# Kernel tuning notes

Hardware: AMD Instinct MI355X
Metric: run time of the kernel (lower is better)

The kernel has to match this reference:

```python
import jax, jax.numpy as jnp
import numpy as np

EPS = 1e-5

def _conv(x, w):
    # 3x3, stride 1, pad 1, NCHW/OIHW
    return jax.lax.conv_general_dilated(x, w, (1, 1), ((1, 1), (1, 1)),
                                        dimension_numbers=('NCHW', 'OIHW', 'NCHW'))

def _bn(x, g, b, m, v):
    inv = jax.lax.rsqrt(v + EPS)
    return (x - m[None, :, None, None]) * (g * inv)[None, :, None, None] + b[None, :, None, None]

def _hardtanh(x):
    return jnp.clip(x, -1.0, 1.0)

def _binarize(x):
    # sign binarization with straight-through estimator (identity gradient)
    s = jnp.where(x >= 0, 1.0, -1.0).astype(x.dtype)
    return x + jax.lax.stop_gradient(s - x)

def _maxpool2(x):
    return jax.lax.reduce_window(x, -jnp.inf, jax.lax.max, (1, 1, 2, 2), (1, 1, 2, 2), 'VALID')

def setup_inputs() -> dict:
    key = jax.random.key(0)
    ks = jax.random.split(key, 8)
    c1, c3, c5 = 128 * 3, 256 * 3, 512 * 3  # infl_ratio = 3
    def W(k, o, i):
        return jax.random.normal(k, (o, i, 3, 3), jnp.float32) * 0.05
    inp = {}
    inp['x'] = jax.random.normal(ks[0], (128, 3, 32, 32), jnp.float32)
    inp['w1'] = W(ks[1], c1, 3)
    inp['w2'] = W(ks[2], c1, c1)
    inp['w3'] = W(ks[3], c3, c1)
    inp['w4'] = W(ks[4], c3, c3)
    inp['w5'] = W(ks[5], c5, c3)
    inp['w6'] = W(ks[6], 512, c5)
    for i, c in zip(range(1, 7), [c1, c1, c3, c3, c5, 512]):
        inp['bn%d_g' % i] = jnp.ones((c,), jnp.float32)
        inp['bn%d_b' % i] = jnp.zeros((c,), jnp.float32)
        inp['bn%d_m' % i] = jnp.zeros((c,), jnp.float32)
        inp['bn%d_v' % i] = jnp.ones((c,), jnp.float32)
    inp['w_lin'] = jax.random.normal(ks[7], (10, 512 * 4 * 4), jnp.float32) * 0.02
    return inp

def reference(x, w1, w2, w3, w4, w5, w6,
              bn1_g, bn1_b, bn1_m, bn1_v,
              bn2_g, bn2_b, bn2_m, bn2_v,
              bn3_g, bn3_b, bn3_m, bn3_v,
              bn4_g, bn4_b, bn4_m, bn4_v,
              bn5_g, bn5_b, bn5_m, bn5_v,
              bn6_g, bn6_b, bn6_m, bn6_v,
              w_lin):
    # block 1: full-precision conv
    h = _hardtanh(_bn(_conv(x, w1), bn1_g, bn1_b, bn1_m, bn1_v))
    # block 2: binarized conv -> maxpool -> BN -> hardtanh
    h = _conv(_binarize(h), _binarize(w2))
    h = _hardtanh(_bn(_maxpool2(h), bn2_g, bn2_b, bn2_m, bn2_v))
    # block 3
    h = _conv(_binarize(h), _binarize(w3))
    h = _hardtanh(_bn(h, bn3_g, bn3_b, bn3_m, bn3_v))
    # block 4
    h = _conv(_binarize(h), _binarize(w4))
    h = _hardtanh(_bn(_maxpool2(h), bn4_g, bn4_b, bn4_m, bn4_v))
    # block 5
    h = _conv(_binarize(h), _binarize(w5))
    h = _hardtanh(_bn(h, bn5_g, bn5_b, bn5_m, bn5_v))
    # block 6
    h = _conv(_binarize(h), _binarize(w6))
    h = _hardtanh(_bn(_maxpool2(h), bn6_g, bn6_b, bn6_m, bn6_v))
    # classifier
    h = h.reshape(-1, 512 * 4 * 4)
    logits = h @ w_lin.T
    return jax.nn.log_softmax(logits, axis=-1)
```

## Files before the change

kernel.cpp:

```cpp
#include <hip/hip_runtime.h>
#include <stdint.h>

#define EPS 1e-5f

typedef __attribute__((ext_vector_type(4))) int i32x4;

__global__ __launch_bounds__(384) void conv1_a1_kernel(
    const float* __restrict__ x,
    const float* __restrict__ w1,
    const float* __restrict__ g,
    const float* __restrict__ b,
    const float* __restrict__ m,
    const float* __restrict__ v,
    char* __restrict__ a1)
{
    const int bid = blockIdx.x;
    const int n = bid >> 2;
    const int q = bid & 3;
    const int tid = threadIdx.x;

    __shared__ float xin[3][10][34];

    const int y0 = q * 8;
    for (int idx = tid; idx < 3 * 10 * 34; idx += 384) {
        int xx = idx % 34;
        int yy = (idx / 34) % 10;
        int ci = idx / 340;
        int gy = y0 - 1 + yy, gx = xx - 1;
        float val = 0.f;
        if (gy >= 0 && gy < 32 && gx >= 0 && gx < 32)
            val = x[((n * 3 + ci) * 32 + gy) * 32 + gx];
        xin[ci][yy][xx] = val;
    }

    float wr[27];
    {
        const float* wp = w1 + tid * 27;
#pragma unroll
        for (int i = 0; i < 27; ++i) wr[i] = wp[i];
    }
    const float scale = g[tid] * rsqrtf(v[tid] + EPS);
    const float mean = m[tid], beta = b[tid];
    __syncthreads();

    for (int yy = 0; yy < 8; ++yy) {
        const int gy = y0 + yy;
        char* orow = a1 + ((size_t)(n * 34 + gy + 1) * 34 + 1) * 384 + tid;
#pragma unroll
        for (int xp = 0; xp < 32; xp += 2) {
            float a0 = 0.f, a1v = 0.f;
#pragma unroll
            for (int ci = 0; ci < 3; ++ci)
#pragma unroll
                for (int dy = 0; dy < 3; ++dy) {
                    float c0 = xin[ci][yy + dy][xp];
                    float c1 = xin[ci][yy + dy][xp + 1];
                    float c2 = xin[ci][yy + dy][xp + 2];
                    float c3 = xin[ci][yy + dy][xp + 3];
                    const float* wrow = &wr[(ci * 3 + dy) * 3];
                    a0 += c0 * wrow[0] + c1 * wrow[1] + c2 * wrow[2];
                    a1v += c1 * wrow[0] + c2 * wrow[1] + c3 * wrow[2];
                }
            float t0 = (a0 - mean) * scale + beta;
            float t1 = (a1v - mean) * scale + beta;
            orow[(size_t)xp * 384] = (t0 >= 0.f) ? 1 : -1;
            orow[(size_t)(xp + 1) * 384] = (t1 >= 0.f) ? 1 : -1;
        }
    }
}

__global__ void pack_bp_kernel(const float* __restrict__ w,
                               char* __restrict__ bp, int Co, int Ci)
{
    int KC = Ci >> 6;
    int idx = blockIdx.x * 256 + threadIdx.x;
    int total = Co * 9 * Ci;
    if (idx >= total) return;
    int t  = idx & 15;
    int fg = (idx >> 4) & 3;
    int co = (idx >> 6) % Co;
    int s  = idx / (Co * 64);
    int tap = s / KC, kc = s % KC;
    int ci = kc * 64 + fg * 16 + t;
    bp[idx] = (w[((size_t)co * Ci + ci) * 9 + tap] >= 0.f) ? 1 : -1;
}

template<int Ci, int Co, int H, int W, int WM, int GN, bool POOL, bool OUTF32>
__global__ __launch_bounds__(WM * 128, 4) void gemm_fused_kernel(
    const char* __restrict__ A,
    const char* __restrict__ Bp,
    const float* __restrict__ g, const float* __restrict__ b,
    const float* __restrict__ m, const float* __restrict__ v,
    char* __restrict__ aout, float* __restrict__ fout)
{
    constexpr int T   = WM * 128;
    constexpr int TM  = WM * 64;
    constexpr int KC  = Ci / 64;
    constexpr int S   = 9 * KC;
    constexpr int WP  = W + 2;
    constexpr int GM  = (128 * H * W) / TM;
    constexpr int BU  = 512 / T;
    constexpr int HO  = POOL ? H / 2 : H;
    constexpr int WO  = POOL ? W / 2 : W;

    __shared__ __align__(16) char lsA[2][TM * 64];
    __shared__ __align__(16) char lsB[2][128 * 64];

    const int id = blockIdx.x;
    const int xcd = id & 7;
    const int s0 = id >> 3;
    const int bm = xcd * (GM / 8) + s0 / GN;
    const int bn = s0 % GN;

    const int tid = threadIdx.x;
    const int lane = tid & 63;
    const int wave = tid >> 6;
    const int wm = wave >> 1, wn = wave & 1;
    const int fr = lane & 15, fg = lane >> 4;

    const int pl = tid >> 1, h = tid & 1;
    int gm = bm * TM + pl;
    int n_  = gm / (H * W);
    int rr = gm % (H * W);
    int y_  = rr / W, x_ = rr % W;
    const char* abase = A + ((size_t)(n_ * (H + 2) + y_) * WP + x_) * Ci + h * 32;
    const int xsw = (pl >> 1) & 3;
    const int wa0 = pl * 64 + (((2 * h) ^ xsw) << 4);
    const int wa1 = pl * 64 + (((2 * h + 1) ^ xsw) << 4);

    const char* bbase = Bp + (size_t)bn * 128 * 64;
    int bdst[BU];
#pragma unroll
    for (int q = 0; q < BU; ++q) {
        int u = tid + q * T;
        int col = u >> 2, sl = u & 3;
        bdst[q] = col * 64 + ((sl ^ ((col >> 1) & 3)) << 4);
    }
    const size_t bstep = (size_t)Co * 64;

    int raA[4];
#pragma unroll
    for (int i = 0; i < 4; ++i) {
        int row = wm * 64 + i * 16 + fr;
        raA[i] = row * 64 + ((fg ^ ((row >> 1) & 3)) << 4);
    }
    int raB[4];
#pragma unroll
    for (int j = 0; j < 4; ++j) {
        int col = wn * 64 + j * 16 + fr;
        raB[j] = col * 64 + ((fg ^ ((col >> 1) & 3)) << 4);
    }

    i32x4 acc[4][4] = {};

    {
        *reinterpret_cast<uint4*>(&lsA[0][wa0]) =
            *reinterpret_cast<const uint4*>(abase);
        *reinterpret_cast<uint4*>(&lsA[0][wa1]) =
            *reinterpret_cast<const uint4*>(abase + 16);
#pragma unroll
        for (int q = 0; q < BU; ++q)
            *reinterpret_cast<uint4*>(&lsB[0][bdst[q]]) =
                *reinterpret_cast<const uint4*>(bbase + (tid + q * T) * 16);
    }
    __syncthreads();

    for (int s = 0; s < S; ++s) {
        const int cur = s & 1;
        const bool more = (s + 1 < S);

        uint4 av0, av1, bst[BU];
        if (more) {
            int s1 = s + 1;
            int tap = s1 / KC, kc = s1 % KC;
            const char* src = abase + ((tap / 3) * WP + (tap % 3)) * Ci + kc * 64;
            av0 = *reinterpret_cast<const uint4*>(src);
            av1 = *reinterpret_cast<const uint4*>(src + 16);
            const char* bsrc = bbase + (size_t)s1 * bstep;
#pragma unroll
            for (int q = 0; q < BU; ++q)
                bst[q] = *reinterpret_cast<const uint4*>(bsrc + (tid + q * T) * 16);
        }

        i32x4 af[4], bf[4];
#pragma unroll
        for (int i = 0; i < 4; ++i)
            af[i] = *reinterpret_cast<const i32x4*>(&lsA[cur][raA[i]]);
#pragma unroll
        for (int j = 0; j < 4; ++j)
            bf[j] = *reinterpret_cast<const i32x4*>(&lsB[cur][raB[j]]);
#pragma unroll
        for (int i = 0; i < 4; ++i)
#pragma unroll
            for (int j = 0; j < 4; ++j)
                acc[i][j] = __builtin_amdgcn_mfma_i32_16x16x64_i8(
                    af[i], bf[j], acc[i][j], 0, 0, 0);

        if (more) {
            *reinterpret_cast<uint4*>(&lsA[cur ^ 1][wa0]) = av0;
            *reinterpret_cast<uint4*>(&lsA[cur ^ 1][wa1]) = av1;
#pragma unroll
            for (int q = 0; q < BU; ++q)
                *reinterpret_cast<uint4*>(&lsB[cur ^ 1][bdst[q]]) = bst[q];
        }
        __syncthreads();
    }

    int colj[4];
    float sc[4], mn[4], bt[4];
#pragma unroll
    for (int j = 0; j < 4; ++j) {
        colj[j] = bn * 128 + wn * 64 + j * 16 + fr;
        sc[j] = g[colj[j]] * rsqrtf(v[colj[j]] + EPS);
        mn[j] = m[colj[j]];
        bt[j] = b[colj[j]];
    }

    if constexpr (POOL && W == 32) {
        const int n = bm >> 2;
        const int Y = 4 * (bm & 3) + wm;
#pragma unroll
        for (int ip = 0; ip < 2; ++ip)
#pragma unroll
            for (int rp = 0; rp < 2; ++rp) {
                int X = ip * 8 + fg * 2 + rp;
#pragma unroll
                for (int j = 0; j < 4; ++j) {
                    int val = max(max(acc[ip][j][2 * rp], acc[ip][j][2 * rp + 1]),
                                  max(acc[ip + 2][j][2 * rp], acc[ip + 2][j][2 * rp + 1]));
                    float t = ((float)val - mn[j]) * sc[j] + bt[j];
                    aout[((size_t)(n * (HO + 2) + Y + 1) * (WO + 2) + X + 1) * Co + colj[j]]
                        = (t >= 0.f) ? 1 : -1;
                }
            }
    } else if constexpr (POOL && W == 16) {
        const int n = bm;
#pragma unroll
        for (int iv = 0; iv < 2; ++iv) {
            int Y = wm * 2 + iv;
#pragma unroll
            for (int rp = 0; rp < 2; ++rp) {
                int X = fg * 2 + rp;
#pragma unroll
                for (int j = 0; j < 4; ++j) {
                    int val = max(max(acc[2 * iv][j][2 * rp], acc[2 * iv][j][2 * rp + 1]),
                                  max(acc[2 * iv + 1][j][2 * rp], acc[2 * iv + 1][j][2 * rp + 1]));
                    float t = ((float)val - mn[j]) * sc[j] + bt[j];
                    aout[((size_t)(n * (HO + 2) + Y + 1) * (WO + 2) + X + 1) * Co + colj[j]]
                        = (t >= 0.f) ? 1 : -1;
                }
            }
        }
    } else if constexpr (POOL && W == 8) {
        const int n = bm * 2 + wm;
#pragma unroll
        for (int i = 0; i < 4; ++i)
#pragma unroll
            for (int rp = 0; rp < 2; ++rp)
#pragma unroll
                for (int j = 0; j < 4; ++j) {
                    int hm = max(acc[i][j][2 * rp], acc[i][j][2 * rp + 1]);
                    int other = __shfl_xor(hm, 32);
                    int val = max(hm, other);
                    if (fg < 2) {
                        int X = (fg & 1) * 2 + rp;
                        float t = ((float)val - mn[j]) * sc[j] + bt[j];
                        t = fminf(1.f, fmaxf(-1.f, t));
                        fout[((size_t)(n * Co + colj[j]) * 4 + i) * 4 + X] = t;
                    }
                }
    } else if constexpr (!POOL && W == 16) {
        const int n = bm;
#pragma unroll
        for (int i = 0; i < 4; ++i) {
            int y = wm * 4 + i;
#pragma unroll
            for (int r = 0; r < 4; ++r) {
                int x = fg * 4 + r;
#pragma unroll
                for (int j = 0; j < 4; ++j) {
                    float t = ((float)acc[i][j][r] - mn[j]) * sc[j] + bt[j];
                    aout[((size_t)(n * (H + 2) + y + 1) * (W + 2) + x + 1) * Co + colj[j]]
                        = (t >= 0.f) ? 1 : -1;
                }
            }
        }
    } else {
        const int n = bm * 2 + wm;
#pragma unroll
        for (int i = 0; i < 4; ++i) {
            int y = 2 * i + (fg >> 1);
#pragma unroll
            for (int r = 0; r < 4; ++r) {
                int x = (fg & 1) * 4 + r;
#pragma unroll
                for (int j = 0; j < 4; ++j) {
                    float t = ((float)acc[i][j][r] - mn[j]) * sc[j] + bt[j];
                    aout[((size_t)(n * (H + 2) + y + 1) * (W + 2) + x + 1) * Co + colj[j]]
                        = (t >= 0.f) ? 1 : -1;
                }
            }
        }
    }
}

__global__ void classifier_kernel(const float* __restrict__ h,
                                  const float* __restrict__ wl,
                                  float* __restrict__ out)
{
    int n = blockIdx.x;
    int tid = threadIdx.x;
    float acc[10];
#pragma unroll
    for (int j = 0; j < 10; ++j) acc[j] = 0.f;
    for (int k = tid; k < 8192; k += 256) {
        float hv = h[n * 8192 + k];
#pragma unroll
        for (int j = 0; j < 10; ++j) acc[j] += hv * wl[j * 8192 + k];
    }
    __shared__ float sred[256];
    __shared__ float logit[10];
    for (int j = 0; j < 10; ++j) {
        sred[tid] = acc[j];
        __syncthreads();
        for (int s = 128; s > 0; s >>= 1) {
            if (tid < s) sred[tid] += sred[tid + s];
            __syncthreads();
        }
        if (tid == 0) logit[j] = sred[0];
        __syncthreads();
    }
    if (tid == 0) {
        float mx = logit[0];
#pragma unroll
        for (int j = 1; j < 10; ++j) mx = fmaxf(mx, logit[j]);
        float s = 0.f;
#pragma unroll
        for (int j = 0; j < 10; ++j) s += expf(logit[j] - mx);
        float lse = logf(s) + mx;
#pragma unroll
        for (int j = 0; j < 10; ++j) out[n * 10 + j] = logit[j] - lse;
    }
}

extern "C" void kernel_launch(void* const* d_in, const int* in_sizes, int n_in,
                              void* d_out, int out_size, void* d_ws, size_t ws_size,
                              hipStream_t stream)
{
    const float* x    = (const float*)d_in[0];
    const float* w1   = (const float*)d_in[1];
    const float* w2   = (const float*)d_in[2];
    const float* w3   = (const float*)d_in[3];
    const float* w4   = (const float*)d_in[4];
    const float* w5   = (const float*)d_in[5];
    const float* w6   = (const float*)d_in[6];
    const float* bn_g[6], *bn_b[6], *bn_m[6], *bn_v[6];
    for (int i = 0; i < 6; ++i) {
        bn_g[i] = (const float*)d_in[7 + i * 4 + 0];
        bn_b[i] = (const float*)d_in[7 + i * 4 + 1];
        bn_m[i] = (const float*)d_in[7 + i * 4 + 2];
        bn_v[i] = (const float*)d_in[7 + i * 4 + 3];
    }
    const float* wlin = (const float*)d_in[31];
    float* out = (float*)d_out;

    const size_t A1 = (size_t)128 * 34 * 34 * 384;
    const size_t A2 = (size_t)128 * 18 * 18 * 384;
    const size_t A3 = (size_t)128 * 18 * 18 * 768;
    const size_t A4 = (size_t)128 * 10 * 10 * 768;
    const size_t A5 = (size_t)128 * 10 * 10 * 1536;
    const size_t SB = A2;
    const size_t SC = A3;
    const size_t H6 = (size_t)128 * 8192 * 4;

    char* ws = (char*)d_ws;
    auto alloc = [&](size_t bytes) {
        char* p = ws;
        ws += (bytes + 255) & ~(size_t)255;
        return p;
    };
    char*  a1 = (char*)alloc(A1);
    char*  sb = (char*)alloc(SB);
    char*  scs = (char*)alloc(SC);
    float* h6 = (float*)alloc(H6);
    char* bp2 = (char*)alloc((size_t)(9 * 6 + 1) * 384 * 64);
    char* bp3 = (char*)alloc((size_t)(9 * 6 + 1) * 768 * 64);
    char* bp4 = (char*)alloc((size_t)(9 * 12 + 1) * 768 * 64);
    char* bp5 = (char*)alloc((size_t)(9 * 12 + 1) * 1536 * 64);
    char* bp6 = (char*)alloc((size_t)(9 * 24 + 1) * 512 * 64);

    char* a2 = sb;
    char* a3 = scs;
    char* a4 = sb;
    char* a5 = scs;

    {
        int t;
        t = 384 * 9 * 384;
        pack_bp_kernel<<<(t + 255) / 256, 256, 0, stream>>>(w2, bp2, 384, 384);
        t = 768 * 9 * 384;
        pack_bp_kernel<<<(t + 255) / 256, 256, 0, stream>>>(w3, bp3, 768, 384);
        t = 768 * 9 * 768;
        pack_bp_kernel<<<(t + 255) / 256, 256, 0, stream>>>(w4, bp4, 768, 768);
        t = 1536 * 9 * 768;
        pack_bp_kernel<<<(t + 255) / 256, 256, 0, stream>>>(w5, bp5, 1536, 768);
        t = 512 * 9 * 1536;
        pack_bp_kernel<<<(t + 255) / 256, 256, 0, stream>>>(w6, bp6, 512, 1536);
    }

    hipMemsetAsync(a1, 0, A1, stream);
    conv1_a1_kernel<<<128 * 4, 384, 0, stream>>>(
        x, w1, bn_g[0], bn_b[0], bn_m[0], bn_v[0], a1);

    hipMemsetAsync(a2, 0, A2, stream);
    gemm_fused_kernel<384, 384, 32, 32, 4, 3, true, false>
        <<<512 * 3, 512, 0, stream>>>(a1, bp2, bn_g[1], bn_b[1], bn_m[1], bn_v[1],
                                      a2, nullptr);
    hipMemsetAsync(a3, 0, A3, stream);
    gemm_fused_kernel<384, 768, 16, 16, 4, 6, false, false>
        <<<128 * 6, 512, 0, stream>>>(a2, bp3, bn_g[2], bn_b[2], bn_m[2], bn_v[2],
                                      a3, nullptr);
    hipMemsetAsync(a4, 0, A4, stream);
    gemm_fused_kernel<768, 768, 16, 16, 4, 6, true, false>
        <<<128 * 6, 512, 0, stream>>>(a3, bp4, bn_g[3], bn_b[3], bn_m[3], bn_v[3],
                                      a4, nullptr);
    hipMemsetAsync(a5, 0, A5, stream);
    gemm_fused_kernel<768, 1536, 8, 8, 2, 12, false, false>
        <<<64 * 12, 256, 0, stream>>>(a4, bp5, bn_g[4], bn_b[4], bn_m[4], bn_v[4],
                                      a5, nullptr);
    gemm_fused_kernel<1536, 512, 8, 8, 2, 4, true, true>
        <<<64 * 4, 256, 0, stream>>>(a5, bp6, bn_g[5], bn_b[5], bn_m[5], bn_v[5],
                                     nullptr, h6);

    classifier_kernel<<<128, 256, 0, stream>>>(h6, wlin, out);
}
```

Measured before the change: 884.1 us.

## Add taller per-wave int8 MFMA GEMM kernel for conv layers 2-4

Adds a new implicit-GEMM kernel in which each of four waves computes a 128x64 output sub-tile (8x4 MFMA fragments) instead of 64x64, keeping the 256x128 block tile but with 256 threads instead of 512. Each wave reuses its B fragments across more A rows, cutting LDS reads per MFMA. The cost is a larger accumulator file (128 VGPRs for acc), with launch bounds relaxed to 2 blocks per CU, and new epilogue index mappings for pooled and unpooled outputs.

```diff
diff --git a/kernel.cpp b/kernel.cpp
--- a/kernel.cpp
+++ b/kernel.cpp
@@ -85,6 +85,195 @@
     bp[idx] = (w[((size_t)co * Ci + ci) * 9 + tap] >= 0.f) ? 1 : -1;
 }
 
+template<int Ci, int Co, int H, int W, int GN, int EPI>
+__global__ __launch_bounds__(256, 2) void gemm_tall_kernel(
+    const char* __restrict__ A,
+    const char* __restrict__ Bp,
+    const float* __restrict__ g, const float* __restrict__ b,
+    const float* __restrict__ m, const float* __restrict__ v,
+    char* __restrict__ aout)
+{
+    constexpr int KC = Ci / 64;
+    constexpr int S  = 9 * KC;
+    constexpr int WP = W + 2;
+    constexpr int GM = (128 * H * W) / 256;
+    constexpr int HO = (EPI != 3) ? H / 2 : H;
+    constexpr int WO = (EPI != 3) ? W / 2 : W;
+
+    __shared__ __align__(16) char lsA[2][256 * 64];
+    __shared__ __align__(16) char lsB[2][128 * 64];
+
+    const int id = blockIdx.x;
+    const int xcd = id & 7;
+    const int s0 = id >> 3;
+    const int bm = xcd * (GM / 8) + s0 / GN;
+    const int bn = s0 % GN;
+
+    const int tid = threadIdx.x;
+    const int lane = tid & 63;
+    const int wave = tid >> 6;
+    const int wm = wave >> 1, wn = wave & 1;
+    const int fr = lane & 15, fg = lane >> 4;
+
+    int gm = bm * 256 + tid;
+    int n_ = gm / (H * W);
+    int rr = gm % (H * W);
+    int y_ = rr / W, x_ = rr % W;
+    const char* abase = A + ((size_t)(n_ * (H + 2) + y_) * WP + x_) * Ci;
+    int wsoA[4];
+#pragma unroll
+    for (int k = 0; k < 4; ++k)
+        wsoA[k] = tid * 64 + ((k ^ ((tid >> 1) & 3)) << 4);
+
+    const char* bbase = Bp + (size_t)bn * 128 * 64;
+    int bdst[2];
+#pragma unroll
+    for (int q = 0; q < 2; ++q) {
+        int u = tid + q * 256;
+        int col = u >> 2, sl = u & 3;
+        bdst[q] = col * 64 + ((sl ^ ((col >> 1) & 3)) << 4);
+    }
+    const size_t bstep = (size_t)Co * 64;
+
+    int raA[8];
+#pragma unroll
+    for (int i = 0; i < 8; ++i) {
+        int row = wm * 128 + i * 16 + fr;
+        raA[i] = row * 64 + ((fg ^ ((row >> 1) & 3)) << 4);
+    }
+    int raB[4];
+#pragma unroll
+    for (int j = 0; j < 4; ++j) {
+        int col = wn * 64 + j * 16 + fr;
+        raB[j] = col * 64 + ((fg ^ ((col >> 1) & 3)) << 4);
+    }
+
+    i32x4 acc[8][4] = {};
+
+    {
+#pragma unroll
+        for (int k = 0; k < 4; ++k)
+            *reinterpret_cast<uint4*>(&lsA[0][wsoA[k]]) =
+                *reinterpret_cast<const uint4*>(abase + k * 16);
+#pragma unroll
+        for (int q = 0; q < 2; ++q)
+            *reinterpret_cast<uint4*>(&lsB[0][bdst[q]]) =
+                *reinterpret_cast<const uint4*>(bbase + (tid + q * 256) * 16);
+    }
+    __syncthreads();
+
+    for (int s = 0; s < S; ++s) {
+        const int cur = s & 1;
+        const bool more = (s + 1 < S);
+
+        uint4 av[4], bst[2];
+        if (more) {
+            int s1 = s + 1;
+            int tap = s1 / KC, kc = s1 % KC;
+            const char* src = abase + ((tap / 3) * WP + (tap % 3)) * Ci + kc * 64;
+#pragma unroll
+            for (int k = 0; k < 4; ++k)
+                av[k] = *reinterpret_cast<const uint4*>(src + k * 16);
+            const char* bsrc = bbase + (size_t)s1 * bstep;
+#pragma unroll
+            for (int q = 0; q < 2; ++q)
+                bst[q] = *reinterpret_cast<const uint4*>(bsrc + (tid + q * 256) * 16);
+        }
+
+        i32x4 af[8], bf[4];
+#pragma unroll
+        for (int i = 0; i < 8; ++i)
+            af[i] = *reinterpret_cast<const i32x4*>(&lsA[cur][raA[i]]);
+#pragma unroll
+        for (int j = 0; j < 4; ++j)
+            bf[j] = *reinterpret_cast<const i32x4*>(&lsB[cur][raB[j]]);
+#pragma unroll
+        for (int i = 0; i < 8; ++i)
+#pragma unroll
+            for (int j = 0; j < 4; ++j)
+                acc[i][j] = __builtin_amdgcn_mfma_i32_16x16x64_i8(
+                    af[i], bf[j], acc[i][j], 0, 0, 0);
+
+        if (more) {
+#pragma unroll
+            for (int k = 0; k < 4; ++k)
+                *reinterpret_cast<uint4*>(&lsA[cur ^ 1][wsoA[k]]) = av[k];
+#pragma unroll
+            for (int q = 0; q < 2; ++q)
+                *reinterpret_cast<uint4*>(&lsB[cur ^ 1][bdst[q]]) = bst[q];
+        }
+        __syncthreads();
+    }
+
+    int colj[4];
+    float sc[4], mn[4], bt[4];
+#pragma unroll
+    for (int j = 0; j < 4; ++j) {
+        colj[j] = bn * 128 + wn * 64 + j * 16 + fr;
+        sc[j] = g[colj[j]] * rsqrtf(v[colj[j]] + EPS);
+        mn[j] = m[colj[j]];
+        bt[j] = b[colj[j]];
+    }
+
+    if constexpr (EPI == 2) {
+        const int n = bm >> 2;
+#pragma unroll
+        for (int ib = 0; ib < 2; ++ib)
+#pragma unroll
+            for (int ix = 0; ix < 2; ++ix) {
+                int i = ib * 4 + ix;
+                int Y = (bm & 3) * 4 + wm * 2 + ib;
+#pragma unroll
+                for (int rp = 0; rp < 2; ++rp) {
+                    int X = ix * 8 + fg * 2 + rp;
+#pragma unroll
+                    for (int j = 0; j < 4; ++j) {
+                        int val = max(max(acc[i][j][2 * rp], acc[i][j][2 * rp + 1]),
+                                      max(acc[i + 2][j][2 * rp], acc[i + 2][j][2 * rp + 1]));
+                        float t = ((float)val - mn[j]) * sc[j] + bt[j];
+                        aout[((size_t)(n * (HO + 2) + Y + 1) * (WO + 2) + X + 1) * Co + colj[j]]
+                            = (t >= 0.f) ? 1 : -1;
+                    }
+                }
+            }
+    } else if constexpr (EPI == 3) {
+        const int n = bm;
+#pragma unroll
+        for (int i = 0; i < 8; ++i) {
+            int y = wm * 8 + i;
+#pragma unroll
+            for (int r = 0; r < 4; ++r) {
+                int x = fg * 4 + r;
+#pragma unroll
+                for (int j = 0; j < 4; ++j) {
+                    float t = ((float)acc[i][j][r] - mn[j]) * sc[j] + bt[j];
+                    aout[((size_t)(n * (H + 2) + y + 1) * (W + 2) + x + 1) * Co + colj[j]]
+                        = (t >= 0.f) ? 1 : -1;
+                }
+            }
+        }
+    } else {
+        const int n = bm;
+#pragma unroll
+        for (int iv = 0; iv < 4; ++iv) {
+            int i = 2 * iv;
+            int Y = wm * 4 + iv;
+#pragma unroll
+            for (int rp = 0; rp < 2; ++rp) {
+                int X = fg * 2 + rp;
+#pragma unroll
+                for (int j = 0; j < 4; ++j) {
+                    int val = max(max(acc[i][j][2 * rp], acc[i][j][2 * rp + 1]),
+                                  max(acc[i + 1][j][2 * rp], acc[i + 1][j][2 * rp + 1]));
+                    float t = ((float)val - mn[j]) * sc[j] + bt[j];
+                    aout[((size_t)(n * (HO + 2) + Y + 1) * (WO + 2) + X + 1) * Co + colj[j]]
+                        = (t >= 0.f) ? 1 : -1;
+                }
+            }
+        }
+    }
+}
+
 template<int Ci, int Co, int H, int W, int WM, int GN, bool POOL, bool OUTF32>
 __global__ __launch_bounds__(WM * 128, 4) void gemm_fused_kernel(
     const char* __restrict__ A,
@@ -100,8 +289,6 @@
     constexpr int WP  = W + 2;
     constexpr int GM  = (128 * H * W) / TM;
     constexpr int BU  = 512 / T;
-    constexpr int HO  = POOL ? H / 2 : H;
-    constexpr int WO  = POOL ? W / 2 : W;
 
     __shared__ __align__(16) char lsA[2][TM * 64];
     __shared__ __align__(16) char lsB[2][128 * 64];
@@ -216,42 +403,7 @@
         bt[j] = b[colj[j]];
     }
 
-    if constexpr (POOL && W == 32) {
-        const int n = bm >> 2;
-        const int Y = 4 * (bm & 3) + wm;
-#pragma unroll
-        for (int ip = 0; ip < 2; ++ip)
-#pragma unroll
-            for (int rp = 0; rp < 2; ++rp) {
-                int X = ip * 8 + fg * 2 + rp;
-#pragma unroll
-                for (int j = 0; j < 4; ++j) {
-                    int val = max(max(acc[ip][j][2 * rp], acc[ip][j][2 * rp + 1]),
-                                  max(acc[ip + 2][j][2 * rp], acc[ip + 2][j][2 * rp + 1]));
-                    float t = ((float)val - mn[j]) * sc[j] + bt[j];
-                    aout[((size_t)(n * (HO + 2) + Y + 1) * (WO + 2) + X + 1) * Co + colj[j]]
-                        = (t >= 0.f) ? 1 : -1;
-                }
-            }
-    } else if constexpr (POOL && W == 16) {
-        const int n = bm;
-#pragma unroll
-        for (int iv = 0; iv < 2; ++iv) {
-            int Y = wm * 2 + iv;
-#pragma unroll
-            for (int rp = 0; rp < 2; ++rp) {
-                int X = fg * 2 + rp;
-#pragma unroll
-                for (int j = 0; j < 4; ++j) {
-                    int val = max(max(acc[2 * iv][j][2 * rp], acc[2 * iv][j][2 * rp + 1]),
-                                  max(acc[2 * iv + 1][j][2 * rp], acc[2 * iv + 1][j][2 * rp + 1]));
-                    float t = ((float)val - mn[j]) * sc[j] + bt[j];
-                    aout[((size_t)(n * (HO + 2) + Y + 1) * (WO + 2) + X + 1) * Co + colj[j]]
-                        = (t >= 0.f) ? 1 : -1;
-                }
-            }
-        }
-    } else if constexpr (POOL && W == 8) {
+    if constexpr (POOL && W == 8) {
         const int n = bm * 2 + wm;
 #pragma unroll
         for (int i = 0; i < 4; ++i)
@@ -269,22 +421,6 @@
                         fout[((size_t)(n * Co + colj[j]) * 4 + i) * 4 + X] = t;
                     }
                 }
-    } else if constexpr (!POOL && W == 16) {
-        const int n = bm;
-#pragma unroll
-        for (int i = 0; i < 4; ++i) {
-            int y = wm * 4 + i;
-#pragma unroll
-            for (int r = 0; r < 4; ++r) {
-                int x = fg * 4 + r;
-#pragma unroll
-                for (int j = 0; j < 4; ++j) {
-                    float t = ((float)acc[i][j][r] - mn[j]) * sc[j] + bt[j];
-                    aout[((size_t)(n * (H + 2) + y + 1) * (W + 2) + x + 1) * Co + colj[j]]
-                        = (t >= 0.f) ? 1 : -1;
-                }
-            }
-        }
     } else {
         const int n = bm * 2 + wm;
 #pragma unroll
@@ -413,17 +549,14 @@
         x, w1, bn_g[0], bn_b[0], bn_m[0], bn_v[0], a1);
 
     hipMemsetAsync(a2, 0, A2, stream);
-    gemm_fused_kernel<384, 384, 32, 32, 4, 3, true, false>
-        <<<512 * 3, 512, 0, stream>>>(a1, bp2, bn_g[1], bn_b[1], bn_m[1], bn_v[1],
-                                      a2, nullptr);
+    gemm_tall_kernel<384, 384, 32, 32, 3, 2>
+        <<<512 * 3, 256, 0, stream>>>(a1, bp2, bn_g[1], bn_b[1], bn_m[1], bn_v[1], a2);
     hipMemsetAsync(a3, 0, A3, stream);
-    gemm_fused_kernel<384, 768, 16, 16, 4, 6, false, false>
-        <<<128 * 6, 512, 0, stream>>>(a2, bp3, bn_g[2], bn_b[2], bn_m[2], bn_v[2],
-                                      a3, nullptr);
+    gemm_tall_kernel<384, 768, 16, 16, 6, 3>
+        <<<128 * 6, 256, 0, stream>>>(a2, bp3, bn_g[2], bn_b[2], bn_m[2], bn_v[2], a3);
     hipMemsetAsync(a4, 0, A4, stream);
-    gemm_fused_kernel<768, 768, 16, 16, 4, 6, true, false>
-        <<<128 * 6, 512, 0, stream>>>(a3, bp4, bn_g[3], bn_b[3], bn_m[3], bn_v[3],
-                                      a4, nullptr);
+    gemm_tall_kernel<768, 768, 16, 16, 6, 4>
+        <<<128 * 6, 256, 0, stream>>>(a3, bp4, bn_g[3], bn_b[3], bn_m[3], bn_v[3], a4);
     hipMemsetAsync(a5, 0, A5, stream);
     gemm_fused_kernel<768, 1536, 8, 8, 2, 12, false, false>
         <<<64 * 12, 256, 0, stream>>>(a4, bp5, bn_g[4], bn_b[4], bn_m[4], bn_v[4],
```

After: 1.052 ms. 1.19x slower.

## Use direct global-to-LDS async loads with triple-buffered pipeline in binary conv GEMM

Applied to the files above, without the earlier changes.

Replaces the register-staged global loads and LDS stores in the int8 MFMA conv GEMM with global_load_lds (direct-to-LDS) transfers. It moves from double to triple buffering with a prefetch distance of two, so loads run further ahead of compute. The full __syncthreads is replaced by explicit vmcnt waits plus s_barrier, and MFMA priority is raised during compute. The cost is more LDS per block, which may lower occupancy, and manual vmcnt counting that depends on the exact number of issued loads.

```diff
diff --git a/kernel.cpp b/kernel.cpp
--- a/kernel.cpp
+++ b/kernel.cpp
@@ -4,6 +4,14 @@
 #define EPS 1e-5f
 
 typedef __attribute__((ext_vector_type(4))) int i32x4;
+
+__device__ __forceinline__ void gload16(const void* g, void* l)
+{
+    __builtin_amdgcn_global_load_lds(
+        (const __attribute__((address_space(1))) void*)g,
+        (__attribute__((address_space(3))) void*)l,
+        16, 0, 0);
+}
 
 __global__ __launch_bounds__(384) void conv1_a1_kernel(
     const float* __restrict__ x,
@@ -85,8 +93,8 @@
     bp[idx] = (w[((size_t)co * Ci + ci) * 9 + tap] >= 0.f) ? 1 : -1;
 }
 
-template<int Ci, int Co, int H, int W, int WM, int GN, bool POOL, bool OUTF32>
-__global__ __launch_bounds__(WM * 128, 4) void gemm_fused_kernel(
+template<int Ci, int Co, int H, int W, int WM, int GN, int EPI>
+__global__ __launch_bounds__(WM * 128, 4) void gemm_async_kernel(
     const char* __restrict__ A,
     const char* __restrict__ Bp,
     const float* __restrict__ g, const float* __restrict__ b,
@@ -100,11 +108,10 @@
     constexpr int WP  = W + 2;
     constexpr int GM  = (128 * H * W) / TM;
     constexpr int BU  = 512 / T;
-    constexpr int HO  = POOL ? H / 2 : H;
-    constexpr int WO  = POOL ? W / 2 : W;
-
-    __shared__ __align__(16) char lsA[2][TM * 64];
-    __shared__ __align__(16) char lsB[2][128 * 64];
+    constexpr int IPS = 2 + BU;
+
+    __shared__ __align__(16) char lsA[3][TM * 64];
+    __shared__ __align__(16) char lsB[3][128 * 64];
 
     const int id = blockIdx.x;
     const int xcd = id & 7;
@@ -118,25 +125,43 @@
     const int wm = wave >> 1, wn = wave & 1;
     const int fr = lane & 15, fg = lane >> 4;
 
-    const int pl = tid >> 1, h = tid & 1;
-    int gm = bm * TM + pl;
-    int n_  = gm / (H * W);
-    int rr = gm % (H * W);
-    int y_  = rr / W, x_ = rr % W;
-    const char* abase = A + ((size_t)(n_ * (H + 2) + y_) * WP + x_) * Ci + h * 32;
-    const int xsw = (pl >> 1) & 3;
-    const int wa0 = pl * 64 + (((2 * h) ^ xsw) << 4);
-    const int wa1 = pl * 64 + (((2 * h + 1) ^ xsw) << 4);
-
-    const char* bbase = Bp + (size_t)bn * 128 * 64;
-    int bdst[BU];
+    const char* asrc[2];
+    int aoff[2];
+#pragma unroll
+    for (int q = 0; q < 2; ++q) {
+        int unit = wave * 128 + q * 64 + lane;
+        int r = unit >> 2, ps = unit & 3;
+        int ls = ps ^ ((r >> 1) & 3);
+        int gm = bm * TM + r;
+        int n_ = gm / (H * W);
+        int rr = gm % (H * W);
+        int y_ = rr / W, x_ = rr % W;
+        asrc[q] = A + ((size_t)(n_ * (H + 2) + y_) * WP + x_) * Ci + ls * 16;
+        aoff[q] = wave * 2048 + q * 1024;
+    }
+    const char* bsrc[BU];
+    int boff[BU];
 #pragma unroll
     for (int q = 0; q < BU; ++q) {
-        int u = tid + q * T;
-        int col = u >> 2, sl = u & 3;
-        bdst[q] = col * 64 + ((sl ^ ((col >> 1) & 3)) << 4);
+        int unit = wave * (64 * BU) + q * 64 + lane;
+        int col = unit >> 2, ps = unit & 3;
+        int ls = ps ^ ((col >> 1) & 3);
+        bsrc[q] = Bp + (size_t)bn * 128 * 64 + col * 64 + ls * 16;
+        boff[q] = wave * (BU * 1024) + q * 1024;
     }
     const size_t bstep = (size_t)Co * 64;
+
+    auto issue = [&](int sx, int t) {
+        int tap = sx / KC, kc = sx % KC;
+        int toff = ((tap / 3) * WP + (tap % 3)) * Ci + kc * 64;
+#pragma unroll
+        for (int q = 0; q < 2; ++q)
+            gload16(asrc[q] + toff, &lsA[t][aoff[q]]);
+        size_t bo = (size_t)sx * bstep;
+#pragma unroll
+        for (int q = 0; q < BU; ++q)
+            gload16(bsrc[q] + bo, &lsB[t][boff[q]]);
+    };
 
     int raA[4];
 #pragma unroll
@@ -153,35 +178,15 @@
 
     i32x4 acc[4][4] = {};
 
-    {
-        *reinterpret_cast<uint4*>(&lsA[0][wa0]) =
-            *reinterpret_cast<const uint4*>(abase);
-        *reinterpret_cast<uint4*>(&lsA[0][wa1]) =
-            *reinterpret_cast<const uint4*>(abase + 16);
-#pragma unroll
-        for (int q = 0; q < BU; ++q)
-            *reinterpret_cast<uint4*>(&lsB[0][bdst[q]]) =
-                *reinterpret_cast<const uint4*>(bbase + (tid + q * T) * 16);
-    }
-    __syncthreads();
-
+    issue(0, 0);
+    issue(1, 1);
+    if constexpr (IPS == 3) asm volatile("s_waitcnt vmcnt(3)" ::: "memory");
+    else                    asm volatile("s_waitcnt vmcnt(4)" ::: "memory");
+    __builtin_amdgcn_sched_barrier(0);
+    __builtin_amdgcn_s_barrier();
+
+    int cur = 0;
     for (int s = 0; s < S; ++s) {
-        const int cur = s & 1;
-        const bool more = (s + 1 < S);
-
-        uint4 av0, av1, bst[BU];
-        if (more) {
-            int s1 = s + 1;
-            int tap = s1 / KC, kc = s1 % KC;
-            const char* src = abase + ((tap / 3) * WP + (tap % 3)) * Ci + kc * 64;
-            av0 = *reinterpret_cast<const uint4*>(src);
-            av1 = *reinterpret_cast<const uint4*>(src + 16);
-            const char* bsrc = bbase + (size_t)s1 * bstep;
-#pragma unroll
-            for (int q = 0; q < BU; ++q)
-                bst[q] = *reinterpret_cast<const uint4*>(bsrc + (tid + q * T) * 16);
-        }
-
         i32x4 af[4], bf[4];
 #pragma unroll
         for (int i = 0; i < 4; ++i)
@@ -189,21 +194,26 @@
 #pragma unroll
         for (int j = 0; j < 4; ++j)
             bf[j] = *reinterpret_cast<const i32x4*>(&lsB[cur][raB[j]]);
+
+        int sx = (s + 2 < S) ? s + 2 : S - 1;
+        int nb = cur + 2; if (nb >= 3) nb -= 3;
+        issue(sx, nb);
+
+        __builtin_amdgcn_s_setprio(1);
 #pragma unroll
         for (int i = 0; i < 4; ++i)
 #pragma unroll
             for (int j = 0; j < 4; ++j)
                 acc[i][j] = __builtin_amdgcn_mfma_i32_16x16x64_i8(
                     af[i], bf[j], acc[i][j], 0, 0, 0);
-
-        if (more) {
-            *reinterpret_cast<uint4*>(&lsA[cur ^ 1][wa0]) = av0;
-            *reinterpret_cast<uint4*>(&lsA[cur ^ 1][wa1]) = av1;
-#pragma unroll
-            for (int q = 0; q < BU; ++q)
-                *reinterpret_cast<uint4*>(&lsB[cur ^ 1][bdst[q]]) = bst[q];
-        }
-        __syncthreads();
+        __builtin_amdgcn_s_setprio(0);
+
+        if constexpr (IPS == 3) asm volatile("s_waitcnt vmcnt(3)" ::: "memory");
+        else                    asm volatile("s_waitcnt vmcnt(4)" ::: "memory");
+        __builtin_amdgcn_sched_barrier(0);
+        __builtin_amdgcn_s_barrier();
+
+        cur = (cur + 1 == 3) ? 0 : cur + 1;
     }
 
     int colj[4];
@@ -216,7 +226,8 @@
         bt[j] = b[colj[j]];
     }
 
-    if constexpr (POOL && W == 32) {
+    if constexpr (EPI == 0) {
+        constexpr int HO = H / 2, WO = W / 2;
         const int n = bm >> 2;
         const int Y = 4 * (bm & 3) + wm;
 #pragma unroll
@@ -233,7 +244,24 @@
                         = (t >= 0.f) ? 1 : -1;
                 }
             }
-    } else if constexpr (POOL && W == 16) {
+    } else if constexpr (EPI == 1) {
+        const int n = bm;
+#pragma unroll
+        for (int i = 0; i < 4; ++i) {
+            int y = wm * 4 + i;
+#pragma unroll
+            for (int r = 0; r < 4; ++r) {
+                int x = fg * 4 + r;
+#pragma unroll
+                for (int j = 0; j < 4; ++j) {
+                    float t = ((float)acc[i][j][r] - mn[j]) * sc[j] + bt[j];
+                    aout[((size_t)(n * (H + 2) + y + 1) * (W + 2) + x + 1) * Co + colj[j]]
+                        = (t >= 0.f) ? 1 : -1;
+                }
+            }
+        }
+    } else if constexpr (EPI == 2) {
+        constexpr int HO = H / 2, WO = W / 2;
         const int n = bm;
 #pragma unroll
         for (int iv = 0; iv < 2; ++iv) {
@@ -251,7 +279,23 @@
                 }
             }
         }
-    } else if constexpr (POOL && W == 8) {
+    } else if constexpr (EPI == 3) {
+        const int n = bm * 2 + wm;
+#pragma unroll
+        for (int i = 0; i < 4; ++i) {
+            int y = 2 * i + (fg >> 1);
+#pragma unroll
+            for (int r = 0; r < 4; ++r) {
+                int x = (fg & 1) * 4 + r;
+#pragma unroll
+                for (int j = 0; j < 4; ++j) {
+                    float t = ((float)acc[i][j][r] - mn[j]) * sc[j] + bt[j];
+                    aout[((size_t)(n * (H + 2) + y + 1) * (W + 2) + x + 1) * Co + colj[j]]
+                        = (t >= 0.f) ? 1 : -1;
+                }
+            }
+        }
+    } else {
         const int n = bm * 2 + wm;
 #pragma unroll
         for (int i = 0; i < 4; ++i)
@@ -269,38 +313,6 @@
                         fout[((size_t)(n * Co + colj[j]) * 4 + i) * 4 + X] = t;
                     }
                 }
-    } else if constexpr (!POOL && W == 16) {
-        const int n = bm;
-#pragma unroll
-        for (int i = 0; i < 4; ++i) {
-            int y = wm * 4 + i;
-#pragma unroll
-            for (int r = 0; r < 4; ++r) {
-                int x = fg * 4 + r;
-#pragma unroll
-                for (int j = 0; j < 4; ++j) {
-                    float t = ((float)acc[i][j][r] - mn[j]) * sc[j] + bt[j];
-                    aout[((size_t)(n * (H + 2) + y + 1) * (W + 2) + x + 1) * Co + colj[j]]
-                        = (t >= 0.f) ? 1 : -1;
-                }
-            }
-        }
-    } else {
-        const int n = bm * 2 + wm;
-#pragma unroll
-        for (int i = 0; i < 4; ++i) {
-            int y = 2 * i + (fg >> 1);
-#pragma unroll
-            for (int r = 0; r < 4; ++r) {
-                int x = (fg & 1) * 4 + r;
-#pragma unroll
-                for (int j = 0; j < 4; ++j) {
-                    float t = ((float)acc[i][j][r] - mn[j]) * sc[j] + bt[j];
-                    aout[((size_t)(n * (H + 2) + y + 1) * (W + 2) + x + 1) * Co + colj[j]]
-                        = (t >= 0.f) ? 1 : -1;
-                }
-            }
-        }
     }
 }
 
@@ -413,22 +425,22 @@
         x, w1, bn_g[0], bn_b[0], bn_m[0], bn_v[0], a1);
 
     hipMemsetAsync(a2, 0, A2, stream);
-    gemm_fused_kernel<384, 384, 32, 32, 4, 3, true, false>
+    gemm_async_kernel<384, 384, 32, 32, 4, 3, 0>
         <<<512 * 3, 512, 0, stream>>>(a1, bp2, bn_g[1], bn_b[1], bn_m[1], bn_v[1],
                                       a2, nullptr);
     hipMemsetAsync(a3, 0, A3, stream);
-    gemm_fused_kernel<384, 768, 16, 16, 4, 6, false, false>
+    gemm_async_kernel<384, 768, 16, 16, 4, 6, 1>
         <<<128 * 6, 512, 0, stream>>>(a2, bp3, bn_g[2], bn_b[2], bn_m[2], bn_v[2],
                                       a3, nullptr);
     hipMemsetAsync(a4, 0, A4, stream);
-    gemm_fused_kernel<768, 768, 16, 16, 4, 6, true, false>
+    gemm_async_kernel<768, 768, 16, 16, 4, 6, 2>
         <<<128 * 6, 512, 0, stream>>>(a3, bp4, bn_g[3], bn_b[3], bn_m[3], bn_v[3],
                                       a4, nullptr);
     hipMemsetAsync(a5, 0, A5, stream);
-    gemm_fused_kernel<768, 1536, 8, 8, 2, 12, false, false>
+    gemm_async_kernel<768, 1536, 8, 8, 2, 12, 3>
         <<<64 * 12, 256, 0, stream>>>(a4, bp5, bn_g[4], bn_b[4], bn_m[4], bn_v[4],
                                       a5, nullptr);
-    gemm_fused_kernel<1536, 512, 8, 8, 2, 4, true, true>
+    gemm_async_kernel<1536, 512, 8, 8, 2, 4, 4>
         <<<64 * 4, 256, 0, stream>>>(a5, bp6, bn_g[5], bn_b[5], bn_m[5], bn_v[5],
                                      nullptr, h6);
 
```

Result: faster. 806.7 us (-8.8%).
